# Kernel optimization log

Measured on AMD Instinct MI355X. Metric: run time of the kernel, lower is better.

## Reference

```python
import jax, jax.numpy as jnp
import numpy as np

NUM_BANDS = 64
LATENT = 256
HIDDEN = 512
G = 8
K = 1024
GD = LATENT // G  # 32
BETA = 0.25


def setup_inputs() -> dict:
    key = jax.random.key(0)
    ks = jax.random.split(key, 10)
    B, T = 16, 1000
    bands = jax.random.normal(ks[0], (B, T, NUM_BANDS), dtype=jnp.float32)
    s = 0.02
    enc_w1 = jax.random.normal(ks[1], (NUM_BANDS, HIDDEN), dtype=jnp.float32) * s
    enc_b1 = jnp.zeros((HIDDEN,), dtype=jnp.float32)
    enc_w2 = jax.random.normal(ks[2], (HIDDEN, LATENT), dtype=jnp.float32) * s
    enc_b2 = jnp.zeros((LATENT,), dtype=jnp.float32)
    codebooks = jax.random.normal(ks[3], (G, K, GD), dtype=jnp.float32) * 0.1
    dec_w1 = jax.random.normal(ks[4], (LATENT, HIDDEN), dtype=jnp.float32) * s
    dec_b1 = jnp.zeros((HIDDEN,), dtype=jnp.float32)
    dec_w2 = jax.random.normal(ks[5], (HIDDEN, NUM_BANDS), dtype=jnp.float32) * s
    dec_b2 = jnp.zeros((NUM_BANDS,), dtype=jnp.float32)
    return {
        "bands": bands,
        "enc_w1": enc_w1, "enc_b1": enc_b1, "enc_w2": enc_w2, "enc_b2": enc_b2,
        "codebooks": codebooks,
        "dec_w1": dec_w1, "dec_b1": dec_b1, "dec_w2": dec_w2, "dec_b2": dec_b2,
    }


def _mlp(x, w1, b1, w2, b2):
    # TimeDistributedMLP: Linear -> ReLU -> Linear applied on last dim
    return jax.nn.relu(x @ w1 + b1) @ w2 + b2


def reference(bands, enc_w1, enc_b1, enc_w2, enc_b2, codebooks,
              dec_w1, dec_b1, dec_w2, dec_b2):
    B, T, _ = bands.shape
    z_e = _mlp(bands, enc_w1, enc_b1, enc_w2, enc_b2)  # (B,T,LATENT)

    # Grouped VQ over flattened frames
    parts = z_e.reshape(B * T, G, GD)                   # (N,G,gd)
    zn = jnp.sum(parts * parts, axis=-1)[:, :, None]    # (N,G,1)
    cn = jnp.sum(codebooks * codebooks, axis=-1)[None]  # (1,G,K)
    cross = jnp.einsum('ngd,gkd->ngk', parts, codebooks)
    dist = zn - 2.0 * cross + cn                        # (N,G,K)
    idx = jnp.argmin(dist, axis=-1)                     # (N,G) int
    z_q = codebooks[jnp.arange(G)[None, :], idx]        # (N,G,gd) gather

    # straight-through estimator
    z_q_st = parts + jax.lax.stop_gradient(z_q - parts)

    # per-group mean losses, summed over groups
    codebook_loss = jnp.sum(jnp.mean((jax.lax.stop_gradient(z_q) - parts) ** 2, axis=(0, 2)))
    commit_loss = jnp.sum(jnp.mean((z_q - jax.lax.stop_gradient(parts)) ** 2, axis=(0, 2)))
    vq_loss = BETA * (codebook_loss + commit_loss)  # epoch=None -> beta_eff = beta

    z_q_out = z_q_st.reshape(B, T, LATENT)
    idx_out = idx.reshape(B, T, G)
    bands_hat = _mlp(z_q_out, dec_w1, dec_b1, dec_w2, dec_b2)
    return (bands_hat, z_e, z_q_out, idx_out, vq_loss)
```

## Files before the change

kernel.cpp:

```cpp
#include <hip/hip_runtime.h>

#define NBANDS 64
#define LATENT 256
#define HIDDEN 512
#define GQ 8
#define KQ 1024
#define GD 32
#define NROWS 16000

#define OUT_BH   0
#define OUT_ZE   1024000
#define OUT_ZQ   5120000
#define OUT_IDX  9216000
#define OUT_LOSS 9344000

#define WS_H     0
#define WS_H2BF_F  0
#define WS_ZQB_F   4096000
#define WS_W1B_F   6144000
#define WS_W2B_F   6209536
#define WS_CBH_F   6240000
#define WS_CBM_F   6400000
#define WS_CBL_F   6560000
#define WS_CN    8192000
#define WS_LOSS  8200192

typedef __attribute__((ext_vector_type(8))) short bf16x8;
typedef __attribute__((ext_vector_type(4))) float f32x4;

__device__ __forceinline__ unsigned short f2bf(float f) {
  unsigned u = __builtin_bit_cast(unsigned, f);
  unsigned r = u + 0x7FFFu + ((u >> 16) & 1u);
  return (unsigned short)(r >> 16);
}

__device__ __forceinline__ float bf2f(unsigned short h) {
  return __builtin_bit_cast(float, ((unsigned)h) << 16);
}

__device__ __forceinline__ void split3(float x, unsigned short& h,
                                       unsigned short& m, unsigned short& l) {
  h = f2bf(x);
  const float r1 = x - bf2f(h);
  m = f2bf(r1);
  const float r2 = r1 - bf2f(m);
  l = f2bf(r2);
}

template<int BN, int TM, int TN, int BK, bool RELU>
__global__ __launch_bounds__(256) void gemm_f32(
    const float* __restrict__ A, const float* __restrict__ B,
    const float* __restrict__ bias, float* __restrict__ C,
    int M, int N, int K) {
  constexpr int BM = 128;
  constexpr int NTX = BN / TN;
  constexpr int AF4 = BK / 8;
  constexpr int QPR = BN / 4;
  constexpr int BF4 = BK * BN / 1024;

  __shared__ float As[BK][BM + 8];
  __shared__ float Bs[BK][BN + 4];

  const int tid = threadIdx.x;
  const int tx = tid % NTX;
  const int ty = tid / NTX;
  const int row0 = blockIdx.y * BM;
  const int col0 = blockIdx.x * BN;

  const int arow = tid >> 1;
  const int akq  = (tid & 1) * (BK / 2);

  float acc[TM][TN] = {};

  for (int k0 = 0; k0 < K; k0 += BK) {
    float4 av[AF4], bv[BF4];
#pragma unroll
    for (int q = 0; q < AF4; ++q)
      av[q] = *reinterpret_cast<const float4*>(
          &A[(size_t)(row0 + arow) * K + k0 + akq + q * 4]);
#pragma unroll
    for (int t = 0; t < BF4; ++t) {
      const int qq = tid * BF4 + t;
      const int bk = qq / QPR, bn4 = qq % QPR;
      bv[t] = *reinterpret_cast<const float4*>(
          &B[(size_t)(k0 + bk) * N + col0 + bn4 * 4]);
    }
    __syncthreads();
#pragma unroll
    for (int q = 0; q < AF4; ++q) {
      As[akq + q * 4 + 0][arow] = av[q].x;
      As[akq + q * 4 + 1][arow] = av[q].y;
      As[akq + q * 4 + 2][arow] = av[q].z;
      As[akq + q * 4 + 3][arow] = av[q].w;
    }
#pragma unroll
    for (int t = 0; t < BF4; ++t) {
      const int qq = tid * BF4 + t;
      const int bk = qq / QPR, bn4 = qq % QPR;
      *reinterpret_cast<float4*>(&Bs[bk][bn4 * 4]) = bv[t];
    }
    __syncthreads();

#pragma unroll
    for (int kk = 0; kk < BK; ++kk) {
      float a[TM], b[TN];
#pragma unroll
      for (int q = 0; q < TM / 4; ++q) {
        float4 v = *reinterpret_cast<const float4*>(&As[kk][ty * TM + q * 4]);
        a[q * 4 + 0] = v.x; a[q * 4 + 1] = v.y;
        a[q * 4 + 2] = v.z; a[q * 4 + 3] = v.w;
      }
#pragma unroll
      for (int q = 0; q < TN / 4; ++q) {
        float4 v = *reinterpret_cast<const float4*>(&Bs[kk][tx * TN + q * 4]);
        b[q * 4 + 0] = v.x; b[q * 4 + 1] = v.y;
        b[q * 4 + 2] = v.z; b[q * 4 + 3] = v.w;
      }
#pragma unroll
      for (int i = 0; i < TM; ++i)
#pragma unroll
        for (int j = 0; j < TN; ++j)
          acc[i][j] = fmaf(a[i], b[j], acc[i][j]);
    }
  }

  float bb[TN];
#pragma unroll
  for (int q = 0; q < TN / 4; ++q) {
    float4 v = *reinterpret_cast<const float4*>(&bias[col0 + tx * TN + q * 4]);
    bb[q * 4 + 0] = v.x; bb[q * 4 + 1] = v.y;
    bb[q * 4 + 2] = v.z; bb[q * 4 + 3] = v.w;
  }
#pragma unroll
  for (int i = 0; i < TM; ++i) {
    const int r = row0 + ty * TM + i;
#pragma unroll
    for (int q = 0; q < TN / 4; ++q) {
      float4 v;
      float* vp = &v.x;
#pragma unroll
      for (int j = 0; j < 4; ++j) {
        float t = acc[i][q * 4 + j] + bb[q * 4 + j];
        if (RELU) t = fmaxf(t, 0.0f);
        vp[j] = t;
      }
      *reinterpret_cast<float4*>(&C[(size_t)r * N + col0 + tx * TN + q * 4]) = v;
    }
  }
}

template<int WM, bool OUT_BF16, bool DO_LOSS>
__global__ __launch_bounds__(256) void gemm_bf16_mfma(
    const unsigned short* __restrict__ A, const unsigned short* __restrict__ BT,
    const float* __restrict__ bias, void* __restrict__ Cout,
    int M, int N, int K,
    const float* __restrict__ loss_acc, float* __restrict__ loss_out) {
  constexpr int BM = 4 * WM;
  constexpr int MT = WM / 16;

  __shared__ unsigned short As[BM][40];
  __shared__ unsigned short Bs[64][40];

  const int tid  = threadIdx.x;
  const int wave = tid >> 6;
  const int lane = tid & 63;
  const int quad = lane >> 4;
  const int l16  = lane & 15;
  const int row0 = blockIdx.y * BM;
  const int col0 = blockIdx.x * 64;

  if (DO_LOSS && blockIdx.x == 0 && blockIdx.y == 0 && tid == 0)
    loss_out[0] = 0.5f * loss_acc[0] / (float)((size_t)NROWS * GD);

  f32x4 acc[MT][4];
#pragma unroll
  for (int mt = 0; mt < MT; ++mt)
#pragma unroll
    for (int nt = 0; nt < 4; ++nt) acc[mt][nt] = (f32x4){0.f, 0.f, 0.f, 0.f};

  for (int k0 = 0; k0 < K; k0 += 32) {
    __syncthreads();
    if constexpr (BM == 128) {
      const int r = tid >> 1, seg = (tid & 1) * 16;
      const uint4* src = reinterpret_cast<const uint4*>(
          &A[(size_t)(row0 + r) * K + k0 + seg]);
      uint4* dst = reinterpret_cast<uint4*>(&As[r][seg]);
      dst[0] = src[0]; dst[1] = src[1];
    } else {
      const int r = tid >> 2, seg = (tid & 3) * 8;
      *reinterpret_cast<uint4*>(&As[r][seg]) =
          *reinterpret_cast<const uint4*>(&A[(size_t)(row0 + r) * K + k0 + seg]);
    }
    {
      const int n = tid >> 2, kc = (tid & 3) * 8;
      *reinterpret_cast<uint4*>(&Bs[n][kc]) =
          *reinterpret_cast<const uint4*>(&BT[(size_t)(col0 + n) * K + k0 + kc]);
    }
    __syncthreads();

    bf16x8 af[MT], bf[4];
#pragma unroll
    for (int mt = 0; mt < MT; ++mt)
      af[mt] = *reinterpret_cast<const bf16x8*>(
          &As[wave * WM + mt * 16 + l16][quad * 8]);
#pragma unroll
    for (int nt = 0; nt < 4; ++nt)
      bf[nt] = *reinterpret_cast<const bf16x8*>(&Bs[nt * 16 + l16][quad * 8]);
#pragma unroll
    for (int mt = 0; mt < MT; ++mt)
#pragma unroll
      for (int nt = 0; nt < 4; ++nt)
        acc[mt][nt] = __builtin_amdgcn_mfma_f32_16x16x32_bf16(
            af[mt], bf[nt], acc[mt][nt], 0, 0, 0);
  }

#pragma unroll
  for (int mt = 0; mt < MT; ++mt)
#pragma unroll
    for (int nt = 0; nt < 4; ++nt) {
      const int col = col0 + nt * 16 + l16;
      const float bv = bias[col];
#pragma unroll
      for (int r = 0; r < 4; ++r) {
        const int grow = row0 + wave * WM + mt * 16 + quad * 4 + r;
        float v = acc[mt][nt][r] + bv;
        if constexpr (OUT_BF16) {
          v = fmaxf(v, 0.0f);
          ((unsigned short*)Cout)[(size_t)grow * N + col] = f2bf(v);
        } else {
          ((float*)Cout)[(size_t)grow * N + col] = v;
        }
      }
    }
}

__global__ void prep_cn(const float* __restrict__ cb, float* __restrict__ cn,
                        float* __restrict__ loss_acc) {
  const int i = blockIdx.x * 256 + threadIdx.x;
  if (i == 0) loss_acc[0] = 0.0f;
  if (i < GQ * KQ) {
    const float* c = cb + (size_t)i * GD;
    float s = 0.0f;
#pragma unroll
    for (int d = 0; d < GD; ++d) s = fmaf(c[d], c[d], s);
    cn[i] = -0.5f * s;
  }
}

__global__ void prep_wT(const float* __restrict__ w1, const float* __restrict__ w2,
                        const float* __restrict__ cbk,
                        unsigned short* __restrict__ w1bT,
                        unsigned short* __restrict__ w2bT,
                        unsigned short* __restrict__ cbh,
                        unsigned short* __restrict__ cbm,
                        unsigned short* __restrict__ cbl) {
  const int t = blockIdx.x * 256 + threadIdx.x;
  if (t < 16384) {
    const int n = t >> 5, k0 = (t & 31) * 8;
    alignas(16) unsigned short o[8];
#pragma unroll
    for (int q = 0; q < 8; ++q) o[q] = f2bf(w1[(size_t)(k0 + q) * HIDDEN + n]);
    *reinterpret_cast<uint4*>(&w1bT[(size_t)n * LATENT + k0]) =
        *reinterpret_cast<const uint4*>(o);
  } else if (t < 20480) {
    const int u = t - 16384;
    const int n = u >> 6, k0 = (u & 63) * 8;
    alignas(16) unsigned short o[8];
#pragma unroll
    for (int q = 0; q < 8; ++q) o[q] = f2bf(w2[(size_t)(k0 + q) * NBANDS + n]);
    *reinterpret_cast<uint4*>(&w2bT[(size_t)n * HIDDEN + k0]) =
        *reinterpret_cast<const uint4*>(o);
  } else if (t < 53248) {
    const int e0 = (t - 20480) * 8;
    alignas(16) unsigned short oh[8], om[8], ol[8];
#pragma unroll
    for (int q = 0; q < 8; ++q) split3(cbk[e0 + q], oh[q], om[q], ol[q]);
    *reinterpret_cast<uint4*>(&cbh[e0]) = *reinterpret_cast<const uint4*>(oh);
    *reinterpret_cast<uint4*>(&cbm[e0]) = *reinterpret_cast<const uint4*>(om);
    *reinterpret_cast<uint4*>(&cbl[e0]) = *reinterpret_cast<const uint4*>(ol);
  }
}

__global__ __launch_bounds__(256, 4) void vq_mfma(
    const float* __restrict__ z_e, const float* __restrict__ cb,
    const float* __restrict__ cnh,
    const unsigned short* __restrict__ cbh,
    const unsigned short* __restrict__ cbm,
    const unsigned short* __restrict__ cbl,
    float* __restrict__ z_q, unsigned short* __restrict__ zqb,
    float* __restrict__ idx_out, float* __restrict__ loss_acc) {
  const int g    = blockIdx.y;
  const int row0 = blockIdx.x * 128;
  const int tid  = threadIdx.x;
  const int wave = tid >> 6;
  const int lane = tid & 63;
  const int quad = lane >> 4;
  const int l16  = lane & 15;

  bf16x8 ah[2], am[2], al[2];
#pragma unroll
  for (int mt = 0; mt < 2; ++mt) {
    const float* zp = &z_e[(size_t)(row0 + wave * 32 + mt * 16 + l16) * LATENT
                           + g * GD + quad * 8];
    const float4 x0 = *reinterpret_cast<const float4*>(zp);
    const float4 x1 = *reinterpret_cast<const float4*>(zp + 4);
    const float xv[8] = {x0.x, x0.y, x0.z, x0.w, x1.x, x1.y, x1.z, x1.w};
    bf16x8 vh, vm, vl;
#pragma unroll
    for (int j = 0; j < 8; ++j) {
      unsigned short sh, sm, sl;
      split3(xv[j], sh, sm, sl);
      vh[j] = (short)sh; vm[j] = (short)sm; vl[j] = (short)sl;
    }
    ah[mt] = vh; am[mt] = vm; al[mt] = vl;
  }

  const size_t cb0 = (size_t)g * KQ * GD;
  const float* cng = cnh + g * KQ;

  float best[8];
  int   bidx[8];
#pragma unroll
  for (int i = 0; i < 8; ++i) { best[i] = -3.0e38f; bidx[i] = 0; }

#pragma unroll 2
  for (int ch = 0; ch < 16; ++ch) {
    bf16x8 Fh[4], Fm[4], Fl[4];
    float  Fc[4];
#pragma unroll
    for (int nt = 0; nt < 4; ++nt) {
      const int code = ch * 64 + nt * 16 + l16;
      const size_t cba = cb0 + (size_t)code * GD + quad * 8;
      Fh[nt] = *reinterpret_cast<const bf16x8*>(&cbh[cba]);
      Fm[nt] = *reinterpret_cast<const bf16x8*>(&cbm[cba]);
      Fl[nt] = *reinterpret_cast<const bf16x8*>(&cbl[cba]);
      Fc[nt] = cng[code];
    }
#pragma unroll
    for (int nt = 0; nt < 4; ++nt) {
      const float c0 = Fc[nt];
      f32x4 a0 = {c0, c0, c0, c0};
      f32x4 a1 = a0;
      a0 = __builtin_amdgcn_mfma_f32_16x16x32_bf16(ah[0], Fh[nt], a0, 0, 0, 0);
      a1 = __builtin_amdgcn_mfma_f32_16x16x32_bf16(ah[1], Fh[nt], a1, 0, 0, 0);
      a0 = __builtin_amdgcn_mfma_f32_16x16x32_bf16(ah[0], Fm[nt], a0, 0, 0, 0);
      a1 = __builtin_amdgcn_mfma_f32_16x16x32_bf16(ah[1], Fm[nt], a1, 0, 0, 0);
      a0 = __builtin_amdgcn_mfma_f32_16x16x32_bf16(am[0], Fh[nt], a0, 0, 0, 0);
      a1 = __builtin_amdgcn_mfma_f32_16x16x32_bf16(am[1], Fh[nt], a1, 0, 0, 0);
      a0 = __builtin_amdgcn_mfma_f32_16x16x32_bf16(ah[0], Fl[nt], a0, 0, 0, 0);
      a1 = __builtin_amdgcn_mfma_f32_16x16x32_bf16(ah[1], Fl[nt], a1, 0, 0, 0);
      a0 = __builtin_amdgcn_mfma_f32_16x16x32_bf16(am[0], Fm[nt], a0, 0, 0, 0);
      a1 = __builtin_amdgcn_mfma_f32_16x16x32_bf16(am[1], Fm[nt], a1, 0, 0, 0);
      a0 = __builtin_amdgcn_mfma_f32_16x16x32_bf16(al[0], Fh[nt], a0, 0, 0, 0);
      a1 = __builtin_amdgcn_mfma_f32_16x16x32_bf16(al[1], Fh[nt], a1, 0, 0, 0);
      const int code = ch * 64 + nt * 16 + l16;
#pragma unroll
      for (int r = 0; r < 4; ++r) {
        if (a0[r] > best[r])     { best[r] = a0[r];     bidx[r] = code; }
        if (a1[r] > best[4 + r]) { best[4 + r] = a1[r]; bidx[4 + r] = code; }
      }
    }
  }

  float sse_local = 0.0f;
#pragma unroll
  for (int s8 = 0; s8 < 8; ++s8) {
    float mb = best[s8];
    int   mi = bidx[s8];
#pragma unroll
    for (int m = 1; m < 16; m <<= 1) {
      const float ov = __shfl_xor(mb, m, 64);
      const int   oi = __shfl_xor(mi, m, 64);
      if (ov > mb || (ov == mb && oi < mi)) { mb = ov; mi = oi; }
    }
    const int mt  = s8 >> 2;
    const int r   = s8 & 3;
    const int row = row0 + wave * 32 + mt * 16 + quad * 4 + r;
    const float2 cw = *reinterpret_cast<const float2*>(
        &cb[cb0 + (size_t)mi * GD + 2 * l16]);
    const float2 zv = *reinterpret_cast<const float2*>(
        &z_e[(size_t)row * LATENT + g * GD + 2 * l16]);
    const float d0 = cw.x - zv.x;
    const float d1 = cw.y - zv.y;
    sse_local = fmaf(d0, d0, fmaf(d1, d1, sse_local));
    *reinterpret_cast<float2*>(
        &z_q[(size_t)row * LATENT + g * GD + 2 * l16]) = cw;
    const unsigned pz = (unsigned)f2bf(cw.x) | ((unsigned)f2bf(cw.y) << 16);
    *reinterpret_cast<unsigned*>(
        &zqb[(size_t)row * LATENT + g * GD + 2 * l16]) = pz;
    if (l16 == 0) idx_out[(size_t)row * GQ + g] = (float)mi;
  }

#pragma unroll
  for (int m = 1; m < 64; m <<= 1) sse_local += __shfl_xor(sse_local, m, 64);
  if (lane == 0) atomicAdd(loss_acc, sse_local);
}

extern "C" void kernel_launch(void* const* d_in, const int* in_sizes, int n_in,
                              void* d_out, int out_size, void* d_ws, size_t ws_size,
                              hipStream_t stream) {
  const float* bands  = (const float*)d_in[0];
  const float* enc_w1 = (const float*)d_in[1];
  const float* enc_b1 = (const float*)d_in[2];
  const float* enc_w2 = (const float*)d_in[3];
  const float* enc_b2 = (const float*)d_in[4];
  const float* cbooks = (const float*)d_in[5];
  const float* dec_w1 = (const float*)d_in[6];
  const float* dec_b1 = (const float*)d_in[7];
  const float* dec_w2 = (const float*)d_in[8];
  const float* dec_b2 = (const float*)d_in[9];

  float* out = (float*)d_out;
  float* ws  = (float*)d_ws;

  float* bands_hat = out + OUT_BH;
  float* z_e       = out + OUT_ZE;
  float* z_q       = out + OUT_ZQ;
  float* idx_f     = out + OUT_IDX;
  float* loss_out  = out + OUT_LOSS;

  float* H        = ws + WS_H;
  float* cn       = ws + WS_CN;
  float* loss_acc = ws + WS_LOSS;
  unsigned short* h2bf = (unsigned short*)(ws + WS_H2BF_F);
  unsigned short* zqb  = (unsigned short*)(ws + WS_ZQB_F);
  unsigned short* w1bT = (unsigned short*)(ws + WS_W1B_F);
  unsigned short* w2bT = (unsigned short*)(ws + WS_W2B_F);
  unsigned short* cbh  = (unsigned short*)(ws + WS_CBH_F);
  unsigned short* cbm  = (unsigned short*)(ws + WS_CBM_F);
  unsigned short* cbl  = (unsigned short*)(ws + WS_CBL_F);

  prep_cn<<<dim3(32), dim3(256), 0, stream>>>(cbooks, cn, loss_acc);

  gemm_f32<128, 8, 8, 16, true ><<<dim3(HIDDEN / 128, NROWS / 128), dim3(256), 0, stream>>>(
      bands, enc_w1, enc_b1, H, NROWS, HIDDEN, NBANDS);
  gemm_f32<64, 4, 8, 32, false><<<dim3(LATENT / 64, NROWS / 128), dim3(256), 0, stream>>>(
      H, enc_w2, enc_b2, z_e, NROWS, LATENT, HIDDEN);

  prep_wT<<<dim3(208), dim3(256), 0, stream>>>(
      dec_w1, dec_w2, cbooks, w1bT, w2bT, cbh, cbm, cbl);

  vq_mfma<<<dim3(NROWS / 128, GQ), dim3(256), 0, stream>>>(
      z_e, cbooks, cn, cbh, cbm, cbl, z_q, zqb, idx_f, loss_acc);

  gemm_bf16_mfma<32, true, true ><<<dim3(HIDDEN / 64, NROWS / 128), dim3(256), 0, stream>>>(
      zqb, w1bT, dec_b1, (void*)h2bf, NROWS, HIDDEN, LATENT, loss_acc, loss_out);
  gemm_bf16_mfma<16, false, false><<<dim3(NBANDS / 64, NROWS / 64), dim3(256), 0, stream>>>(
      h2bf, w2bT, dec_b2, (void*)bands_hat, NROWS, NBANDS, HIDDEN, loss_acc, loss_out);
}
```

Measured before the change: 294.0 us.

## Double-buffer codebook loads and interleave independent MFMA chains in VQ kernel

Restructures the VQ argmin loop into a software pipeline with two register buffers, so the codebook fragments for the next chunk load while the current chunk computes. The MFMA sequence is reordered to run across 8 independent accumulators instead of two dependent chains per tile, which exposes more instruction-level parallelism. Launch bounds drop from 4 to 2 blocks per SM to make room for the extra registers, at the cost of lower occupancy.

```diff
diff --git a/kernel.cpp b/kernel.cpp
--- a/kernel.cpp
+++ b/kernel.cpp
@@ -281,7 +281,76 @@
   }
 }
 
-__global__ __launch_bounds__(256, 4) void vq_mfma(
+__device__ __forceinline__ void vq_load(
+    const unsigned short* __restrict__ cbh,
+    const unsigned short* __restrict__ cbm,
+    const unsigned short* __restrict__ cbl,
+    const float* __restrict__ cng, size_t cb0, int ch, int l16, int quad,
+    bf16x8 (&Fh)[4], bf16x8 (&Fm)[4], bf16x8 (&Fl)[4], float (&Fc)[4]) {
+#pragma unroll
+  for (int nt = 0; nt < 4; ++nt) {
+    const int code = ch * 64 + nt * 16 + l16;
+    const size_t cba = cb0 + (size_t)code * GD + quad * 8;
+    Fh[nt] = *reinterpret_cast<const bf16x8*>(&cbh[cba]);
+    Fm[nt] = *reinterpret_cast<const bf16x8*>(&cbm[cba]);
+    Fl[nt] = *reinterpret_cast<const bf16x8*>(&cbl[cba]);
+    Fc[nt] = cng[code];
+  }
+}
+
+__device__ __forceinline__ void vq_compute(
+    const bf16x8 (&ah)[2], const bf16x8 (&am)[2], const bf16x8 (&al)[2],
+    const bf16x8 (&Fh)[4], const bf16x8 (&Fm)[4], const bf16x8 (&Fl)[4],
+    const float (&Fc)[4], int ch, int l16,
+    float (&best)[8], int (&bidx)[8]) {
+  f32x4 acc[8];
+#pragma unroll
+  for (int nt = 0; nt < 4; ++nt) {
+    acc[2 * nt]     = (f32x4){Fc[nt], Fc[nt], Fc[nt], Fc[nt]};
+    acc[2 * nt + 1] = acc[2 * nt];
+  }
+#pragma unroll
+  for (int nt = 0; nt < 4; ++nt) {
+    acc[2*nt]   = __builtin_amdgcn_mfma_f32_16x16x32_bf16(ah[0], Fh[nt], acc[2*nt],   0, 0, 0);
+    acc[2*nt+1] = __builtin_amdgcn_mfma_f32_16x16x32_bf16(ah[1], Fh[nt], acc[2*nt+1], 0, 0, 0);
+  }
+#pragma unroll
+  for (int nt = 0; nt < 4; ++nt) {
+    acc[2*nt]   = __builtin_amdgcn_mfma_f32_16x16x32_bf16(ah[0], Fm[nt], acc[2*nt],   0, 0, 0);
+    acc[2*nt+1] = __builtin_amdgcn_mfma_f32_16x16x32_bf16(ah[1], Fm[nt], acc[2*nt+1], 0, 0, 0);
+  }
+#pragma unroll
+  for (int nt = 0; nt < 4; ++nt) {
+    acc[2*nt]   = __builtin_amdgcn_mfma_f32_16x16x32_bf16(am[0], Fh[nt], acc[2*nt],   0, 0, 0);
+    acc[2*nt+1] = __builtin_amdgcn_mfma_f32_16x16x32_bf16(am[1], Fh[nt], acc[2*nt+1], 0, 0, 0);
+  }
+#pragma unroll
+  for (int nt = 0; nt < 4; ++nt) {
+    acc[2*nt]   = __builtin_amdgcn_mfma_f32_16x16x32_bf16(ah[0], Fl[nt], acc[2*nt],   0, 0, 0);
+    acc[2*nt+1] = __builtin_amdgcn_mfma_f32_16x16x32_bf16(ah[1], Fl[nt], acc[2*nt+1], 0, 0, 0);
+  }
+#pragma unroll
+  for (int nt = 0; nt < 4; ++nt) {
+    acc[2*nt]   = __builtin_amdgcn_mfma_f32_16x16x32_bf16(am[0], Fm[nt], acc[2*nt],   0, 0, 0);
+    acc[2*nt+1] = __builtin_amdgcn_mfma_f32_16x16x32_bf16(am[1], Fm[nt], acc[2*nt+1], 0, 0, 0);
+  }
+#pragma unroll
+  for (int nt = 0; nt < 4; ++nt) {
+    acc[2*nt]   = __builtin_amdgcn_mfma_f32_16x16x32_bf16(al[0], Fh[nt], acc[2*nt],   0, 0, 0);
+    acc[2*nt+1] = __builtin_amdgcn_mfma_f32_16x16x32_bf16(al[1], Fh[nt], acc[2*nt+1], 0, 0, 0);
+  }
+#pragma unroll
+  for (int nt = 0; nt < 4; ++nt) {
+    const int code = ch * 64 + nt * 16 + l16;
+#pragma unroll
+    for (int r = 0; r < 4; ++r) {
+      if (acc[2*nt][r]   > best[r])     { best[r]     = acc[2*nt][r];   bidx[r]     = code; }
+      if (acc[2*nt+1][r] > best[4 + r]) { best[4 + r] = acc[2*nt+1][r]; bidx[4 + r] = code; }
+    }
+  }
+}
+
+__global__ __launch_bounds__(256, 2) void vq_mfma(
     const float* __restrict__ z_e, const float* __restrict__ cb,
     const float* __restrict__ cnh,
     const unsigned short* __restrict__ cbh,
@@ -323,43 +392,16 @@
 #pragma unroll
   for (int i = 0; i < 8; ++i) { best[i] = -3.0e38f; bidx[i] = 0; }
 
-#pragma unroll 2
-  for (int ch = 0; ch < 16; ++ch) {
-    bf16x8 Fh[4], Fm[4], Fl[4];
-    float  Fc[4];
-#pragma unroll
-    for (int nt = 0; nt < 4; ++nt) {
-      const int code = ch * 64 + nt * 16 + l16;
-      const size_t cba = cb0 + (size_t)code * GD + quad * 8;
-      Fh[nt] = *reinterpret_cast<const bf16x8*>(&cbh[cba]);
-      Fm[nt] = *reinterpret_cast<const bf16x8*>(&cbm[cba]);
-      Fl[nt] = *reinterpret_cast<const bf16x8*>(&cbl[cba]);
-      Fc[nt] = cng[code];
-    }
-#pragma unroll
-    for (int nt = 0; nt < 4; ++nt) {
-      const float c0 = Fc[nt];
-      f32x4 a0 = {c0, c0, c0, c0};
-      f32x4 a1 = a0;
-      a0 = __builtin_amdgcn_mfma_f32_16x16x32_bf16(ah[0], Fh[nt], a0, 0, 0, 0);
-      a1 = __builtin_amdgcn_mfma_f32_16x16x32_bf16(ah[1], Fh[nt], a1, 0, 0, 0);
-      a0 = __builtin_amdgcn_mfma_f32_16x16x32_bf16(ah[0], Fm[nt], a0, 0, 0, 0);
-      a1 = __builtin_amdgcn_mfma_f32_16x16x32_bf16(ah[1], Fm[nt], a1, 0, 0, 0);
-      a0 = __builtin_amdgcn_mfma_f32_16x16x32_bf16(am[0], Fh[nt], a0, 0, 0, 0);
-      a1 = __builtin_amdgcn_mfma_f32_16x16x32_bf16(am[1], Fh[nt], a1, 0, 0, 0);
-      a0 = __builtin_amdgcn_mfma_f32_16x16x32_bf16(ah[0], Fl[nt], a0, 0, 0, 0);
-      a1 = __builtin_amdgcn_mfma_f32_16x16x32_bf16(ah[1], Fl[nt], a1, 0, 0, 0);
-      a0 = __builtin_amdgcn_mfma_f32_16x16x32_bf16(am[0], Fm[nt], a0, 0, 0, 0);
-      a1 = __builtin_amdgcn_mfma_f32_16x16x32_bf16(am[1], Fm[nt], a1, 0, 0, 0);
-      a0 = __builtin_amdgcn_mfma_f32_16x16x32_bf16(al[0], Fh[nt], a0, 0, 0, 0);
-      a1 = __builtin_amdgcn_mfma_f32_16x16x32_bf16(al[1], Fh[nt], a1, 0, 0, 0);
-      const int code = ch * 64 + nt * 16 + l16;
-#pragma unroll
-      for (int r = 0; r < 4; ++r) {
-        if (a0[r] > best[r])     { best[r] = a0[r];     bidx[r] = code; }
-        if (a1[r] > best[4 + r]) { best[4 + r] = a1[r]; bidx[4 + r] = code; }
-      }
-    }
+  bf16x8 Xh[4], Xm[4], Xl[4]; float Xc[4];
+  bf16x8 Yh[4], Ym[4], Yl[4]; float Yc[4];
+  vq_load(cbh, cbm, cbl, cng, cb0, 0, l16, quad, Xh, Xm, Xl, Xc);
+#pragma unroll 1
+  for (int cp = 0; cp < 8; ++cp) {
+    vq_load(cbh, cbm, cbl, cng, cb0, 2 * cp + 1, l16, quad, Yh, Ym, Yl, Yc);
+    vq_compute(ah, am, al, Xh, Xm, Xl, Xc, 2 * cp, l16, best, bidx);
+    if (cp < 7)
+      vq_load(cbh, cbm, cbl, cng, cb0, 2 * cp + 2, l16, quad, Xh, Xm, Xl, Xc);
+    vq_compute(ah, am, al, Yh, Ym, Yl, Yc, 2 * cp + 1, l16, best, bidx);
   }
 
   float sse_local = 0.0f;
```

Result: no change. 288.8 us (-1.8%).
